# Kernel optimization log

Hardware: AMD Instinct MI355X
Metric: run time of the kernel (lower is better)

Reference implementation:

```python
import math
import jax, jax.numpy as jnp
import numpy as np

B, S, D = 4, 2048, 1024
H, HD = 16, 64
NUM_BUCKETS = 32
MAX_DISTANCE = 128
EPS = 1e-6
ENC_S = 512


def _relative_position_bucket(relative_position):
    # bidirectional=False path
    num_buckets = NUM_BUCKETS
    rp = -jnp.minimum(relative_position, 0)  # [S, S] nonneg
    max_exact = num_buckets // 2
    is_small = rp < max_exact
    scale = (num_buckets - max_exact) / math.log(MAX_DISTANCE / max_exact)
    large = max_exact + (jnp.log(jnp.maximum(rp, 1).astype(jnp.float32) / max_exact) * scale).astype(jnp.int32)
    large = jnp.minimum(large, num_buckets - 1)
    return jnp.where(is_small, rp, large)


def compute_bias(rel_emb, q_len, k_len):
    ctx = jnp.arange(q_len)[:, None]
    mem = jnp.arange(k_len)[None, :]
    bucket = _relative_position_bucket(mem - ctx)          # [q, k] int
    values = rel_emb[bucket]                                # [q, k, H]
    return jnp.transpose(values, (2, 0, 1))[None]           # [1, H, q, k]


def setup_inputs() -> dict:
    key = jax.random.key(0)
    ks = jax.random.split(key, 8)
    std = 0.02
    return {
        "input_ids": jax.random.normal(ks[0], (B, S, D), jnp.float32),
        "encoder_output": jax.random.normal(ks[1], (B, ENC_S, D), jnp.float32),
        "wq": jax.random.normal(ks[2], (D, H * HD), jnp.float32) * std,
        "wk": jax.random.normal(ks[3], (D, H * HD), jnp.float32) * std,
        "wv": jax.random.normal(ks[4], (D, H * HD), jnp.float32) * std,
        "wo": jax.random.normal(ks[5], (H * HD, D), jnp.float32) * std,
        "rel_emb": jax.random.normal(ks[6], (NUM_BUCKETS, H), jnp.float32) * std,
        "ln_w": jnp.ones((D,), jnp.float32),
    }


def reference(input_ids, encoder_output, wq, wk, wv, wo, rel_emb, ln_w):
    origin = input_ids
    # MT5LayerNorm: RMS norm, no mean subtraction, no bias
    variance = jnp.mean(jnp.square(input_ids.astype(jnp.float32)), axis=-1, keepdims=True)
    x = (input_ids * jax.lax.rsqrt(variance + EPS)) * ln_w

    q = (x @ wq).reshape(B, S, H, HD)
    k = (x @ wk).reshape(B, S, H, HD)
    v = (x @ wv).reshape(B, S, H, HD)

    # NOTE: T5-style attention has no 1/sqrt(d) scaling
    scores = jnp.einsum("bqhd,bkhd->bhqk", q, k)
    scores = scores + compute_bias(rel_emb, S, S)
    attn = jax.nn.softmax(scores, axis=-1)
    ctx = jnp.einsum("bhqk,bkhd->bqhd", attn, v).reshape(B, S, H * HD)
    attn_out = ctx @ wo

    # residual connection (dropout is identity at rate 0 / eval)
    return origin + attn_out
```

## Files before the change

### kernel.cpp

```cpp
#include <hip/hip_runtime.h>
#include <hip/hip_bf16.h>
#include <math.h>

#define S_LEN 2048
#define D_DIM 1024
#define NHEAD 16

typedef __attribute__((ext_vector_type(8))) short bf16x8;
typedef __attribute__((ext_vector_type(4))) float floatx4;

__device__ __forceinline__ short f32_bf16(float f) {
  union { float f; unsigned u; } v; v.f = f;
  unsigned r = v.u + 0x7FFFu + ((v.u >> 16) & 1u);
  return (short)(r >> 16);
}

__device__ __forceinline__ float exp2_fast(float x) {
#if __has_builtin(__builtin_amdgcn_exp2f)
  return __builtin_amdgcn_exp2f(x);
#else
  float r; asm("v_exp_f32 %0, %1" : "=v"(r) : "v"(x)); return r;
#endif
}

__device__ __forceinline__ void gload16(const void* g, void* l) {
  __builtin_amdgcn_global_load_lds((const __attribute__((address_space(1))) unsigned*)g,
                                   (__attribute__((address_space(3))) unsigned*)l,
                                   16, 0, 0);
}

__global__ __launch_bounds__(256) void prep_k(const float* __restrict__ x,
                                              const float* __restrict__ lnw,
                                              const float* __restrict__ wq,
                                              const float* __restrict__ wk,
                                              const float* __restrict__ wv,
                                              const float* __restrict__ wo,
                                              short* __restrict__ xb,
                                              short* __restrict__ oqkv,
                                              short* __restrict__ owo) {
  if (blockIdx.x < 8192) {
    int row = blockIdx.x;
    const float4* xr = (const float4*)(x + (size_t)row * D_DIM);
    float4 v = xr[threadIdx.x];
    float ss = v.x*v.x + v.y*v.y + v.z*v.z + v.w*v.w;
    #pragma unroll
    for (int off = 32; off > 0; off >>= 1) ss += __shfl_xor(ss, off);
    __shared__ float red[4];
    if ((threadIdx.x & 63) == 0) red[threadIdx.x >> 6] = ss;
    __syncthreads();
    float scale = rsqrtf((red[0]+red[1]+red[2]+red[3]) * (1.f/D_DIM) + 1e-6f);
    float4 wv4 = ((const float4*)lnw)[threadIdx.x];
    short4 o;
    o.x = f32_bf16(v.x*scale*wv4.x);
    o.y = f32_bf16(v.y*scale*wv4.y);
    o.z = f32_bf16(v.z*scale*wv4.z);
    o.w = f32_bf16(v.w*scale*wv4.w);
    ((short4*)xb)[(size_t)row*256 + threadIdx.x] = o;
  } else {
    __shared__ float tile[64][65];
    int id = blockIdx.x - 8192;
    int m  = id >> 8;
    int tt = id & 255;
    int tn = tt >> 4, tk = tt & 15;
    const float* src = (m == 0) ? wq : (m == 1) ? wk : (m == 2) ? wv : wo;
    float scale = (m == 0) ? 1.44269504f : 1.0f;
    int t = threadIdx.x;
    int kl  = t >> 4;
    int nl4 = t & 15;
    #pragma unroll
    for (int i = 0; i < 4; i++) {
      int k = i*16 + kl;
      float4 v = *(const float4*)&src[(size_t)(tk*64 + k)*1024 + tn*64 + nl4*4];
      tile[k][nl4*4+0] = v.x;
      tile[k][nl4*4+1] = v.y;
      tile[k][nl4*4+2] = v.z;
      tile[k][nl4*4+3] = v.w;
    }
    __syncthreads();
    short* dst = (m < 3) ? oqkv : owo;
    size_t nbase = (m < 3) ? (size_t)m * 1024 : 0;
    #pragma unroll
    for (int i = 0; i < 2; i++) {
      int idx = i*256 + t;
      int nl = idx >> 3;
      int g  = idx & 7;
      short tmp[8];
      #pragma unroll
      for (int j = 0; j < 8; j++) tmp[j] = f32_bf16(tile[g*8 + j][nl] * scale);
      *(bf16x8*)&dst[(nbase + tn*64 + nl)*1024 + tk*64 + g*8] = *(bf16x8*)tmp;
    }
  }
}

template<bool WRITE_VT>
__global__ __launch_bounds__(512, 2) void gemm256(const short* __restrict__ A,
                                                  const short* __restrict__ Bt,
                                                  short* __restrict__ Cb,
                                                  short* __restrict__ vt,
                                                  int N, int K, int NBN) {
  __shared__ __align__(16) short As[4][256*32];
  __shared__ __align__(16) short Bs[4][256*32];
  const int tid = threadIdx.x;
  const int w = tid >> 6, lane = tid & 63, quad = lane >> 4, l16 = lane & 15;
  const int wm = w >> 2, wn = w & 3;
  const int id = blockIdx.x;
  const int o = (id & 7) * (gridDim.x >> 3) + (id >> 3);
  const int bm = o / NBN, bn = o % NBN;
  const short* Ag = A  + (size_t)bm * 256 * K;
  const short* Bg = Bt + (size_t)bn * 256 * K;
  const int r4 = lane >> 2, c4 = lane & 3;
  const int lc  = c4 ^ ((r4 >> 1) & 3);
  const int swz = (quad ^ ((l16 >> 1) & 3)) * 8;

  floatx4 acc[8][4] = {};

  #define SA(t_) do {                                                          \
    gload16(Ag + (size_t)((w    )*16 + r4) * K + (size_t)(t_)*32 + lc*8,       \
            &As[(t_) & 3][(w    )*512]);                                       \
    gload16(Ag + (size_t)((w + 8)*16 + r4) * K + (size_t)(t_)*32 + lc*8,       \
            &As[(t_) & 3][(w + 8)*512]);                                       \
  } while (0)
  #define SB(t_) do {                                                          \
    gload16(Bg + (size_t)((w    )*16 + r4) * K + (size_t)(t_)*32 + lc*8,       \
            &Bs[(t_) & 3][(w    )*512]);                                       \
    gload16(Bg + (size_t)((w + 8)*16 + r4) * K + (size_t)(t_)*32 + lc*8,       \
            &Bs[(t_) & 3][(w + 8)*512]);                                       \
  } while (0)

  #define PH(t_, STG_, VMW_) do {                                              \
    const short* Ab = &As[(t_) & 3][0];                                        \
    const short* Bb = &Bs[(t_) & 3][0];                                        \
    bf16x8 af[8], bfr[4];                                                      \
    _Pragma("unroll")                                                          \
    for (int i = 0; i < 8; i++)                                                \
      af[i] = *(const bf16x8*)&Ab[(wm*128 + i*16 + l16)*32 + swz];             \
    bfr[0] = *(const bf16x8*)&Bb[(wn*64 +  0 + l16)*32 + swz];                 \
    bfr[1] = *(const bf16x8*)&Bb[(wn*64 + 16 + l16)*32 + swz];                 \
    if (STG_) SA((t_) + 3);                                                    \
    asm volatile("s_waitcnt lgkmcnt(0)");                                      \
    __builtin_amdgcn_sched_barrier(0);                                         \
    __builtin_amdgcn_s_setprio(1);                                             \
    _Pragma("unroll")                                                          \
    for (int i = 0; i < 8; i++) {                                              \
      acc[i][0] = __builtin_amdgcn_mfma_f32_16x16x32_bf16(af[i], bfr[0], acc[i][0], 0, 0, 0); \
      acc[i][1] = __builtin_amdgcn_mfma_f32_16x16x32_bf16(af[i], bfr[1], acc[i][1], 0, 0, 0); \
    }                                                                          \
    __builtin_amdgcn_s_setprio(0);                                             \
    bfr[2] = *(const bf16x8*)&Bb[(wn*64 + 32 + l16)*32 + swz];                 \
    bfr[3] = *(const bf16x8*)&Bb[(wn*64 + 48 + l16)*32 + swz];                 \
    if (STG_) SB((t_) + 3);                                                    \
    asm volatile("s_waitcnt lgkmcnt(0)");                                      \
    __builtin_amdgcn_sched_barrier(0);                                         \
    __builtin_amdgcn_s_setprio(1);                                             \
    _Pragma("unroll")                                                          \
    for (int i = 0; i < 8; i++) {                                              \
      acc[i][2] = __builtin_amdgcn_mfma_f32_16x16x32_bf16(af[i], bfr[2], acc[i][2], 0, 0, 0); \
      acc[i][3] = __builtin_amdgcn_mfma_f32_16x16x32_bf16(af[i], bfr[3], acc[i][3], 0, 0, 0); \
    }                                                                          \
    __builtin_amdgcn_s_setprio(0);                                             \
    asm volatile("s_waitcnt " VMW_);                                           \
    __builtin_amdgcn_s_barrier();                                              \
    __builtin_amdgcn_sched_barrier(0);                                         \
  } while (0)

  SA(0); SB(0); SA(1); SB(1); SA(2); SB(2);
  asm volatile("s_waitcnt vmcnt(8)");
  __builtin_amdgcn_s_barrier();
  __builtin_amdgcn_sched_barrier(0);

  #pragma unroll 1
  for (int t = 0; t < 29; ++t) PH(t, true, "vmcnt(8)");
  PH(29, false, "vmcnt(4)");
  PH(30, false, "vmcnt(0)");
  PH(31, false, "vmcnt(0)");
  #undef SA
  #undef SB
  #undef PH

  if (WRITE_VT && (bn*256 + wn*64) >= 2048) {
    #pragma unroll
    for (int i = 0; i < 8; i++) {
      int row0 = bm*256 + wm*128 + i*16 + quad*4;
      int b = row0 >> 11, s = row0 & 2047;
      #pragma unroll
      for (int j = 0; j < 4; j++) {
        int hcol = bn*256 + wn*64 + j*16 + l16 - 2048;
        short4 st;
        st.x = f32_bf16(acc[i][j][0]);
        st.y = f32_bf16(acc[i][j][1]);
        st.z = f32_bf16(acc[i][j][2]);
        st.w = f32_bf16(acc[i][j][3]);
        int bh = (b << 4) + (hcol >> 6);
        *(short4*)&vt[((size_t)(bh*64 + (hcol & 63)))*2048 + s] = st;
      }
    }
    return;
  }

  #pragma unroll
  for (int i = 0; i < 8; i++) {
    int row0 = bm*256 + wm*128 + i*16 + quad*4;
    #pragma unroll
    for (int j = 0; j < 4; j++) {
      int col = bn*256 + wn*64 + j*16 + l16;
      #pragma unroll
      for (int r = 0; r < 4; r++)
        Cb[(size_t)(row0 + r) * N + col] = f32_bf16(acc[i][j][r]);
    }
  }
}

template<bool ADD_RES, int PANELS>
__global__ __launch_bounds__(256) void gemm_bt(const short* __restrict__ A,
                                               const short* __restrict__ Bt,
                                               short* __restrict__ Cb,
                                               float* __restrict__ Cf,
                                               const float* __restrict__ res,
                                               int M, int N, int K) {
  constexpr int BK = 32;
  __shared__ __align__(16) short As[2][128*BK];
  __shared__ __align__(16) short Bs[2][128*BK];
  int tid = threadIdx.x;
  int w = tid >> 6, lane = tid & 63, quad = lane >> 4, l16 = lane & 15;
  int wr = w >> 1, wc = w & 1;
  const int id = blockIdx.x;
  const int xcd = id & 7, g = id >> 3;
  const int bm = g / PANELS;
  const int bn = xcd * PANELS + (g % PANELS);
  const short* Ag = A + (size_t)bm * 128 * K;
  const short* Bg = Bt + (size_t)bn * 128 * K;
  const int r4 = lane >> 2;
  const int c4 = lane & 3;
  const int lc = c4 ^ ((r4 >> 1) & 3);
  const int swz = (quad ^ ((l16 >> 1) & 3)) * 8;

  floatx4 acc[4][4] = {};

  #define GSTAGE(p_, k0_) do {                                                  \
    _Pragma("unroll")                                                           \
    for (int i = 0; i < 2; i++) {                                               \
      int c = w + i*4;                                                          \
      gload16(Ag + (size_t)(c*16 + r4) * K + (k0_) + lc*8, &As[p_][c*16*BK]);   \
      gload16(Bg + (size_t)(c*16 + r4) * K + (k0_) + lc*8, &Bs[p_][c*16*BK]);   \
    }                                                                           \
  } while (0)

  GSTAGE(0, 0);
  int p = 0;
  for (int k0 = 0; k0 < K; k0 += BK) {
    __syncthreads();
    if (k0 + BK < K) GSTAGE(p ^ 1, k0 + BK);
    bf16x8 af[4], bfr[4];
    #pragma unroll
    for (int i = 0; i < 4; i++) {
      af[i]  = *(const bf16x8*)&As[p][(wr*64 + i*16 + l16)*BK + swz];
      bfr[i] = *(const bf16x8*)&Bs[p][(wc*64 + i*16 + l16)*BK + swz];
    }
    #pragma unroll
    for (int i = 0; i < 4; i++)
      #pragma unroll
      for (int j = 0; j < 4; j++)
        acc[i][j] = __builtin_amdgcn_mfma_f32_16x16x32_bf16(af[i], bfr[j], acc[i][j], 0, 0, 0);
    p ^= 1;
  }
  #undef GSTAGE

  #pragma unroll
  for (int i = 0; i < 4; i++) {
    int row0 = bm*128 + wr*64 + i*16 + quad*4;
    #pragma unroll
    for (int j = 0; j < 4; j++) {
      int col = bn*128 + wc*64 + j*16 + l16;
      #pragma unroll
      for (int r = 0; r < 4; r++) {
        size_t idx = (size_t)(row0 + r) * N + col;
        if (ADD_RES) Cf[idx] = res[idx] + acc[i][j][r];
        else         Cb[idx] = f32_bf16(acc[i][j][r]);
      }
    }
  }
}

__global__ __launch_bounds__(512) void flash_k(const short* __restrict__ qkv,
                                               const short* __restrict__ vt,
                                               const float* __restrict__ rel_emb,
                                               short* __restrict__ ctx) {
  __shared__ __align__(16) short Kb[2][64*64];
  __shared__ __align__(16) short Vb[2][64*64];
  __shared__ float lut2[132];

  const int L = blockIdx.x + 8*blockIdx.y;
  const int xcd = L & 7, kk_ = L >> 3;
  const int bh = xcd*8 + (kk_ >> 3);
  const int qt = kk_ & 7;
  const int b = bh >> 4, h = bh & 15;
  const int t = threadIdx.x, w = t >> 6, lane = t & 63, quad = lane >> 4, l16 = lane & 15;
  const float L2E = 1.44269504f;

  if (t < 129) {
    int rp = t, bucket;
    if (rp < 16) bucket = rp;
    else {
      bucket = 16 + (int)(logf((float)rp * 0.0625f) * (16.f / logf(8.f)));
      if (bucket > 31) bucket = 31;
    }
    lut2[t] = rel_emb[bucket*16 + h] * L2E;
  }
  const float bfut  = rel_emb[h] * L2E;
  const float bpast = rel_emb[31*16 + h] * L2E;
  const floatx4 bf4 = {bfut, bfut, bfut, bfut};
  const floatx4 bp4 = {bpast, bpast, bpast, bpast};
  const floatx4 zz4 = {0.f, 0.f, 0.f, 0.f};

  const int srow = lane >> 3;
  const int slc  = (lane & 7) ^ srow;
  const int rho  = w*8 + srow;
  const int kperm = 32*(rho >> 5) + 8*((rho >> 2) & 3) + 4*((rho >> 4) & 1) + (rho & 3);

  const short* kgU = qkv + ((size_t)b*S_LEN)*3072 + 1024 + h*64;
  const int    loK = kperm*3072 + slc*8;
  const short* vgU = vt + ((size_t)bh*64)*2048;
  const int    loV = rho*2048 + slc*8;

  bf16x8 qB[2][2];
  #pragma unroll
  for (int rb = 0; rb < 2; rb++) {
    const short* qb = qkv + ((size_t)(b*S_LEN + qt*256 + rb*128 + w*16 + l16))*3072 + h*64;
    qB[rb][0] = *(const bf16x8*)&qb[quad*8];
    qB[rb][1] = *(const bf16x8*)&qb[32 + quad*8];
  }

  floatx4 o[2][4] = {};
  floatx4 li4[2] = {};
  const short ONE = (short)0x3F80;
  bf16x8 onesA = {ONE, ONE, ONE, ONE, ONE, ONE, ONE, ONE};

  const int swz0 = (quad     ^ (l16 & 7)) * 8;
  const int swz1 = ((quad+4) ^ (l16 & 7)) * 8;

  #define STAGE(P_, KT_) do {                                                   \
    const short* ka_ = kgU + (size_t)(KT_)*196608 + loK;                        \
    gload16(ka_, &Kb[P_][(w*8)*64]);                                            \
    const short* va_ = vgU + loV + (KT_)*64;                                    \
    gload16(va_, &Vb[P_][(w*8)*64]);                                            \
  } while (0)

  #define BODY(P_, KT_) do {                                                    \
    __syncthreads();                                                            \
    if ((KT_) < 31) STAGE((P_) ^ 1, (KT_) + 1);                                 \
    bool boundary = ((KT_) >= 4*qt - 2) && ((KT_) <= 4*qt + 3);                 \
    floatx4 cinit = boundary ? zz4 : (((KT_) >= 4*qt) ? bf4 : bp4);             \
    floatx4 sc[2][4];                                                           \
    _Pragma("unroll")                                                           \
    for (int c = 0; c < 4; c++) {                                               \
      int rowA = (c*16 + l16)*64;                                               \
      bf16x8 ka0 = *(const bf16x8*)&Kb[P_][rowA + swz0];                        \
      bf16x8 ka1 = *(const bf16x8*)&Kb[P_][rowA + swz1];                        \
      _Pragma("unroll")                                                         \
      for (int rb = 0; rb < 2; rb++) {                                          \
        floatx4 z = __builtin_amdgcn_mfma_f32_16x16x32_bf16(ka0, qB[rb][0], cinit, 0, 0, 0); \
        z = __builtin_amdgcn_mfma_f32_16x16x32_bf16(ka1, qB[rb][1], z, 0, 0, 0);\
        sc[rb][c] = z;                                                          \
      }                                                                         \
    }                                                                           \
    if (boundary) {                                                             \
      _Pragma("unroll")                                                         \
      for (int rb = 0; rb < 2; rb++) {                                          \
        int q0 = qt*256 + rb*128 + w*16 + l16;                                  \
        _Pragma("unroll")                                                       \
        for (int c = 0; c < 4; c++) {                                           \
          int kk = (KT_)*64 + 32*(c >> 1) + 8*quad + 4*(c & 1);                 \
          _Pragma("unroll")                                                     \
          for (int r = 0; r < 4; r++) {                                         \
            int d = q0 - (kk + r);                                              \
            d = d < 0 ? 0 : (d > 128 ? 128 : d);                                \
            sc[rb][c][r] += lut2[d];                                            \
          }                                                                     \
        }                                                                       \
      }                                                                         \
    }                                                                           \
    _Pragma("unroll")                                                           \
    for (int rb = 0; rb < 2; rb++)                                              \
      _Pragma("unroll")                                                         \
      for (int c = 0; c < 4; c++)                                               \
        _Pragma("unroll")                                                       \
        for (int r = 0; r < 4; r++)                                             \
          sc[rb][c][r] = exp2_fast(sc[rb][c][r]);                               \
    bf16x8 pf[2][2];                                                            \
    _Pragma("unroll")                                                           \
    for (int rb = 0; rb < 2; rb++) {                                            \
      _Pragma("unroll")                                                         \
      for (int hh = 0; hh < 2; hh++) {                                          \
        union { bf16x8 v; unsigned u[4]; } pk;                                  \
        floatx4 a = sc[rb][2*hh], bb = sc[rb][2*hh + 1];                        \
        pk.u[0] = __builtin_amdgcn_perm(__float_as_uint(a[1]),  __float_as_uint(a[0]),  0x07060302); \
        pk.u[1] = __builtin_amdgcn_perm(__float_as_uint(a[3]),  __float_as_uint(a[2]),  0x07060302); \
        pk.u[2] = __builtin_amdgcn_perm(__float_as_uint(bb[1]), __float_as_uint(bb[0]), 0x07060302); \
        pk.u[3] = __builtin_amdgcn_perm(__float_as_uint(bb[3]), __float_as_uint(bb[2]), 0x07060302); \
        pf[rb][hh] = pk.v;                                                      \
      }                                                                         \
    }                                                                           \
    _Pragma("unroll")                                                           \
    for (int rb = 0; rb < 2; rb++) {                                            \
      li4[rb] = __builtin_amdgcn_mfma_f32_16x16x32_bf16(onesA, pf[rb][0], li4[rb], 0, 0, 0); \
      li4[rb] = __builtin_amdgcn_mfma_f32_16x16x32_bf16(onesA, pf[rb][1], li4[rb], 0, 0, 0); \
    }                                                                           \
    _Pragma("unroll")                                                           \
    for (int jj = 0; jj < 4; jj++) {                                            \
      int rowV = (jj*16 + l16)*64;                                              \
      bf16x8 va0 = *(const bf16x8*)&Vb[P_][rowV + swz0];                        \
      bf16x8 va1 = *(const bf16x8*)&Vb[P_][rowV + swz1];                        \
      _Pragma("unroll")                                                         \
      for (int rb = 0; rb < 2; rb++) {                                          \
        o[rb][jj] = __builtin_amdgcn_mfma_f32_16x16x32_bf16(va0, pf[rb][0], o[rb][jj], 0, 0, 0); \
        o[rb][jj] = __builtin_amdgcn_mfma_f32_16x16x32_bf16(va1, pf[rb][1], o[rb][jj], 0, 0, 0); \
      }                                                                         \
    }                                                                           \
  } while (0)

  STAGE(0, 0);
  for (int kt = 0; kt < 32; kt += 2) {
    BODY(0, kt);
    BODY(1, kt + 1);
  }

  #pragma unroll
  for (int rb = 0; rb < 2; rb++) {
    float inv = 1.f / li4[rb][0];
    size_t row = (size_t)(b*S_LEN + qt*256 + rb*128 + w*16 + l16);
    #pragma unroll
    for (int jj = 0; jj < 4; jj++) {
      short4 st;
      st.x = f32_bf16(o[rb][jj][0] * inv);
      st.y = f32_bf16(o[rb][jj][1] * inv);
      st.z = f32_bf16(o[rb][jj][2] * inv);
      st.w = f32_bf16(o[rb][jj][3] * inv);
      *(short4*)&ctx[row*1024 + h*64 + jj*16 + quad*4] = st;
    }
  }
  #undef STAGE
  #undef BODY
}

extern "C" void kernel_launch(void* const* d_in, const int* in_sizes, int n_in,
                              void* d_out, int out_size, void* d_ws, size_t ws_size,
                              hipStream_t stream) {
  const float* input_ids = (const float*)d_in[0];
  const float* wq      = (const float*)d_in[2];
  const float* wk      = (const float*)d_in[3];
  const float* wv      = (const float*)d_in[4];
  const float* wo      = (const float*)d_in[5];
  const float* rel_emb = (const float*)d_in[6];
  const float* ln_w    = (const float*)d_in[7];
  float* out = (float*)d_out;

  char* ws = (char*)d_ws;
  short* xb     = (short*)ws;  ws += (size_t)8192*1024*2;
  short* wqkv_t = (short*)ws;  ws += (size_t)3072*1024*2;
  short* wo_t   = (short*)ws;  ws += (size_t)1024*1024*2;
  short* qkv    = (short*)ws;  ws += (size_t)8192*3072*2;
  short* vt     = (short*)ws;  ws += (size_t)64*64*2048*2;
  short* ctx    = (short*)ws;  ws += (size_t)8192*1024*2;

  prep_k<<<8192 + 1024, 256, 0, stream>>>(input_ids, ln_w, wq, wk, wv, wo,
                                          xb, wqkv_t, wo_t);
  gemm256<true><<<384, 512, 0, stream>>>(xb, wqkv_t, qkv, vt, 3072, 1024, 12);
  flash_k<<<dim3(8, 64), 512, 0, stream>>>(qkv, vt, rel_emb, ctx);
  gemm_bt<true, 1><<<512, 256, 0, stream>>>(ctx, wo_t, nullptr, out, input_ids,
                                            8192, 1024, 1024);
}
```

Measured before the change: 284.0 us.

## Shrink gemm256 to 256x128 tiles, reuse it for output projection, software-pipeline PV

The QKV GEMM tile narrows from 256x256 to 256x128, doubling the grid to 768 blocks and halving B-side shared memory and accumulators. The same kernel, with a residual-add epilogue, replaces the separate 128x128 output-projection GEMM. In the flash kernel, P·V for tile k-1 now runs while tile k's softmax is produced, using a third V buffer and a final drain step, so exp/pack work overlaps with MFMA. Costs are more A-tile reloads, extra registers for the previous P fragments, and a triple-buffer rotation that adds bookkeeping.

```diff
diff --git a/kernel.cpp b/kernel.cpp
--- a/kernel.cpp
+++ b/kernel.cpp
@@ -92,71 +92,65 @@
   }
 }
 
-template<bool WRITE_VT>
-__global__ __launch_bounds__(512, 2) void gemm256(const short* __restrict__ A,
-                                                  const short* __restrict__ Bt,
-                                                  short* __restrict__ Cb,
-                                                  short* __restrict__ vt,
-                                                  int N, int K, int NBN) {
+template<bool WRITE_VT, bool ADD_RES>
+__global__ __launch_bounds__(512) void gemm256(const short* __restrict__ A,
+                                               const short* __restrict__ Bt,
+                                               short* __restrict__ Cb,
+                                               float* __restrict__ Cf,
+                                               const float* __restrict__ res,
+                                               short* __restrict__ vt,
+                                               int N, int NBN) {
   __shared__ __align__(16) short As[4][256*32];
-  __shared__ __align__(16) short Bs[4][256*32];
+  __shared__ __align__(16) short Bs[4][128*32];
   const int tid = threadIdx.x;
   const int w = tid >> 6, lane = tid & 63, quad = lane >> 4, l16 = lane & 15;
   const int wm = w >> 2, wn = w & 3;
   const int id = blockIdx.x;
   const int o = (id & 7) * (gridDim.x >> 3) + (id >> 3);
   const int bm = o / NBN, bn = o % NBN;
-  const short* Ag = A  + (size_t)bm * 256 * K;
-  const short* Bg = Bt + (size_t)bn * 256 * K;
+  const short* Ag = A  + (size_t)bm * 256 * 1024;
+  const short* Bg = Bt + (size_t)bn * 128 * 1024;
   const int r4 = lane >> 2, c4 = lane & 3;
   const int lc  = c4 ^ ((r4 >> 1) & 3);
   const int swz = (quad ^ ((l16 >> 1) & 3)) * 8;
 
-  floatx4 acc[8][4] = {};
+  floatx4 acc[8][2] = {};
 
   #define SA(t_) do {                                                          \
-    gload16(Ag + (size_t)((w    )*16 + r4) * K + (size_t)(t_)*32 + lc*8,       \
+    gload16(Ag + (size_t)((w    )*16 + r4) * 1024 + (t_)*32 + lc*8,            \
             &As[(t_) & 3][(w    )*512]);                                       \
-    gload16(Ag + (size_t)((w + 8)*16 + r4) * K + (size_t)(t_)*32 + lc*8,       \
+    gload16(Ag + (size_t)((w + 8)*16 + r4) * 1024 + (t_)*32 + lc*8,            \
             &As[(t_) & 3][(w + 8)*512]);                                       \
   } while (0)
   #define SB(t_) do {                                                          \
-    gload16(Bg + (size_t)((w    )*16 + r4) * K + (size_t)(t_)*32 + lc*8,       \
+    gload16(Bg + (size_t)((w    )*16 + r4) * 1024 + (t_)*32 + lc*8,            \
             &Bs[(t_) & 3][(w    )*512]);                                       \
-    gload16(Bg + (size_t)((w + 8)*16 + r4) * K + (size_t)(t_)*32 + lc*8,       \
-            &Bs[(t_) & 3][(w + 8)*512]);                                       \
   } while (0)
 
   #define PH(t_, STG_, VMW_) do {                                              \
     const short* Ab = &As[(t_) & 3][0];                                        \
     const short* Bb = &Bs[(t_) & 3][0];                                        \
-    bf16x8 af[8], bfr[4];                                                      \
+    bf16x8 af[8], bf0, bf1;                                                    \
     _Pragma("unroll")                                                          \
     for (int i = 0; i < 8; i++)                                                \
       af[i] = *(const bf16x8*)&Ab[(wm*128 + i*16 + l16)*32 + swz];             \
-    bfr[0] = *(const bf16x8*)&Bb[(wn*64 +  0 + l16)*32 + swz];                 \
-    bfr[1] = *(const bf16x8*)&Bb[(wn*64 + 16 + l16)*32 + swz];                 \
+    bf0 = *(const bf16x8*)&Bb[(wn*32 +  0 + l16)*32 + swz];                    \
     if (STG_) SA((t_) + 3);                                                    \
     asm volatile("s_waitcnt lgkmcnt(0)");                                      \
     __builtin_amdgcn_sched_barrier(0);                                         \
     __builtin_amdgcn_s_setprio(1);                                             \
     _Pragma("unroll")                                                          \
-    for (int i = 0; i < 8; i++) {                                              \
-      acc[i][0] = __builtin_amdgcn_mfma_f32_16x16x32_bf16(af[i], bfr[0], acc[i][0], 0, 0, 0); \
-      acc[i][1] = __builtin_amdgcn_mfma_f32_16x16x32_bf16(af[i], bfr[1], acc[i][1], 0, 0, 0); \
-    }                                                                          \
+    for (int i = 0; i < 8; i++)                                                \
+      acc[i][0] = __builtin_amdgcn_mfma_f32_16x16x32_bf16(af[i], bf0, acc[i][0], 0, 0, 0); \
     __builtin_amdgcn_s_setprio(0);                                             \
-    bfr[2] = *(const bf16x8*)&Bb[(wn*64 + 32 + l16)*32 + swz];                 \
-    bfr[3] = *(const bf16x8*)&Bb[(wn*64 + 48 + l16)*32 + swz];                 \
+    bf1 = *(const bf16x8*)&Bb[(wn*32 + 16 + l16)*32 + swz];                    \
     if (STG_) SB((t_) + 3);                                                    \
     asm volatile("s_waitcnt lgkmcnt(0)");                                      \
     __builtin_amdgcn_sched_barrier(0);                                         \
     __builtin_amdgcn_s_setprio(1);                                             \
     _Pragma("unroll")                                                          \
-    for (int i = 0; i < 8; i++) {                                              \
-      acc[i][2] = __builtin_amdgcn_mfma_f32_16x16x32_bf16(af[i], bfr[2], acc[i][2], 0, 0, 0); \
-      acc[i][3] = __builtin_amdgcn_mfma_f32_16x16x32_bf16(af[i], bfr[3], acc[i][3], 0, 0, 0); \
-    }                                                                          \
+    for (int i = 0; i < 8; i++)                                                \
+      acc[i][1] = __builtin_amdgcn_mfma_f32_16x16x32_bf16(af[i], bf1, acc[i][1], 0, 0, 0); \
     __builtin_amdgcn_s_setprio(0);                                             \
     asm volatile("s_waitcnt " VMW_);                                           \
     __builtin_amdgcn_s_barrier();                                              \
@@ -164,27 +158,27 @@
   } while (0)
 
   SA(0); SB(0); SA(1); SB(1); SA(2); SB(2);
-  asm volatile("s_waitcnt vmcnt(8)");
+  asm volatile("s_waitcnt vmcnt(6)");
   __builtin_amdgcn_s_barrier();
   __builtin_amdgcn_sched_barrier(0);
 
   #pragma unroll 1
-  for (int t = 0; t < 29; ++t) PH(t, true, "vmcnt(8)");
-  PH(29, false, "vmcnt(4)");
+  for (int t = 0; t < 29; ++t) PH(t, true, "vmcnt(6)");
+  PH(29, false, "vmcnt(3)");
   PH(30, false, "vmcnt(0)");
   PH(31, false, "vmcnt(0)");
   #undef SA
   #undef SB
   #undef PH
 
-  if (WRITE_VT && (bn*256 + wn*64) >= 2048) {
+  if (WRITE_VT && bn >= 16) {
     #pragma unroll
     for (int i = 0; i < 8; i++) {
       int row0 = bm*256 + wm*128 + i*16 + quad*4;
       int b = row0 >> 11, s = row0 & 2047;
       #pragma unroll
-      for (int j = 0; j < 4; j++) {
-        int hcol = bn*256 + wn*64 + j*16 + l16 - 2048;
+      for (int j = 0; j < 2; j++) {
+        int hcol = (bn - 16)*128 + wn*32 + j*16 + l16;
         short4 st;
         st.x = f32_bf16(acc[i][j][0]);
         st.y = f32_bf16(acc[i][j][1]);
@@ -201,76 +195,8 @@
   for (int i = 0; i < 8; i++) {
     int row0 = bm*256 + wm*128 + i*16 + quad*4;
     #pragma unroll
-    for (int j = 0; j < 4; j++) {
-      int col = bn*256 + wn*64 + j*16 + l16;
-      #pragma unroll
-      for (int r = 0; r < 4; r++)
-        Cb[(size_t)(row0 + r) * N + col] = f32_bf16(acc[i][j][r]);
-    }
-  }
-}
-
-template<bool ADD_RES, int PANELS>
-__global__ __launch_bounds__(256) void gemm_bt(const short* __restrict__ A,
-                                               const short* __restrict__ Bt,
-                                               short* __restrict__ Cb,
-                                               float* __restrict__ Cf,
-                                               const float* __restrict__ res,
-                                               int M, int N, int K) {
-  constexpr int BK = 32;
-  __shared__ __align__(16) short As[2][128*BK];
-  __shared__ __align__(16) short Bs[2][128*BK];
-  int tid = threadIdx.x;
-  int w = tid >> 6, lane = tid & 63, quad = lane >> 4, l16 = lane & 15;
-  int wr = w >> 1, wc = w & 1;
-  const int id = blockIdx.x;
-  const int xcd = id & 7, g = id >> 3;
-  const int bm = g / PANELS;
-  const int bn = xcd * PANELS + (g % PANELS);
-  const short* Ag = A + (size_t)bm * 128 * K;
-  const short* Bg = Bt + (size_t)bn * 128 * K;
-  const int r4 = lane >> 2;
-  const int c4 = lane & 3;
-  const int lc = c4 ^ ((r4 >> 1) & 3);
-  const int swz = (quad ^ ((l16 >> 1) & 3)) * 8;
-
-  floatx4 acc[4][4] = {};
-
-  #define GSTAGE(p_, k0_) do {                                                  \
-    _Pragma("unroll")                                                           \
-    for (int i = 0; i < 2; i++) {                                               \
-      int c = w + i*4;                                                          \
-      gload16(Ag + (size_t)(c*16 + r4) * K + (k0_) + lc*8, &As[p_][c*16*BK]);   \
-      gload16(Bg + (size_t)(c*16 + r4) * K + (k0_) + lc*8, &Bs[p_][c*16*BK]);   \
-    }                                                                           \
-  } while (0)
-
-  GSTAGE(0, 0);
-  int p = 0;
-  for (int k0 = 0; k0 < K; k0 += BK) {
-    __syncthreads();
-    if (k0 + BK < K) GSTAGE(p ^ 1, k0 + BK);
-    bf16x8 af[4], bfr[4];
-    #pragma unroll
-    for (int i = 0; i < 4; i++) {
-      af[i]  = *(const bf16x8*)&As[p][(wr*64 + i*16 + l16)*BK + swz];
-      bfr[i] = *(const bf16x8*)&Bs[p][(wc*64 + i*16 + l16)*BK + swz];
-    }
-    #pragma unroll
-    for (int i = 0; i < 4; i++)
-      #pragma unroll
-      for (int j = 0; j < 4; j++)
-        acc[i][j] = __builtin_amdgcn_mfma_f32_16x16x32_bf16(af[i], bfr[j], acc[i][j], 0, 0, 0);
-    p ^= 1;
-  }
-  #undef GSTAGE
-
-  #pragma unroll
-  for (int i = 0; i < 4; i++) {
-    int row0 = bm*128 + wr*64 + i*16 + quad*4;
-    #pragma unroll
-    for (int j = 0; j < 4; j++) {
-      int col = bn*128 + wc*64 + j*16 + l16;
+    for (int j = 0; j < 2; j++) {
+      int col = bn*128 + wn*32 + j*16 + l16;
       #pragma unroll
       for (int r = 0; r < 4; r++) {
         size_t idx = (size_t)(row0 + r) * N + col;
@@ -286,7 +212,7 @@
                                                const float* __restrict__ rel_emb,
                                                short* __restrict__ ctx) {
   __shared__ __align__(16) short Kb[2][64*64];
-  __shared__ __align__(16) short Vb[2][64*64];
+  __shared__ __align__(16) short Vb[3][64*64];
   __shared__ float lut2[132];
 
   const int L = blockIdx.x + 8*blockIdx.y;
@@ -322,6 +248,11 @@
   const short* vgU = vt + ((size_t)bh*64)*2048;
   const int    loV = rho*2048 + slc*8;
 
+  {
+    bf16x8 z = {};
+    *(bf16x8*)&Vb[2][t*8] = z;
+  }
+
   bf16x8 qB[2][2];
   #pragma unroll
   for (int rb = 0; rb < 2; rb++) {
@@ -334,20 +265,24 @@
   floatx4 li4[2] = {};
   const short ONE = (short)0x3F80;
   bf16x8 onesA = {ONE, ONE, ONE, ONE, ONE, ONE, ONE, ONE};
+  bf16x8 pfP[2][2] = {};
 
   const int swz0 = (quad     ^ (l16 & 7)) * 8;
   const int swz1 = ((quad+4) ^ (l16 & 7)) * 8;
 
-  #define STAGE(P_, KT_) do {                                                   \
+  int vnext = 1;
+  int vprev = 2;
+
+  #define STAGE_T(KP_, VN_, KT_) do {                                           \
     const short* ka_ = kgU + (size_t)(KT_)*196608 + loK;                        \
-    gload16(ka_, &Kb[P_][(w*8)*64]);                                            \
+    gload16(ka_, &Kb[KP_][(w*8)*64]);                                           \
     const short* va_ = vgU + loV + (KT_)*64;                                    \
-    gload16(va_, &Vb[P_][(w*8)*64]);                                            \
+    gload16(va_, &Vb[VN_][(w*8)*64]);                                           \
   } while (0)
 
   #define BODY(P_, KT_) do {                                                    \
     __syncthreads();                                                            \
-    if ((KT_) < 31) STAGE((P_) ^ 1, (KT_) + 1);                                 \
+    if ((KT_) < 31) STAGE_T((P_) ^ 1, vnext, (KT_) + 1);                        \
     bool boundary = ((KT_) >= 4*qt - 2) && ((KT_) <= 4*qt + 3);                 \
     floatx4 cinit = boundary ? zz4 : (((KT_) >= 4*qt) ? bf4 : bp4);             \
     floatx4 sc[2][4];                                                           \
@@ -386,7 +321,7 @@
         _Pragma("unroll")                                                       \
         for (int r = 0; r < 4; r++)                                             \
           sc[rb][c][r] = exp2_fast(sc[rb][c][r]);                               \
-    bf16x8 pf[2][2];                                                            \
+    bf16x8 pfL[2][2];                                                           \
     _Pragma("unroll")                                                           \
     for (int rb = 0; rb < 2; rb++) {                                            \
       _Pragma("unroll")                                                         \
@@ -397,31 +332,51 @@
         pk.u[1] = __builtin_amdgcn_perm(__float_as_uint(a[3]),  __float_as_uint(a[2]),  0x07060302); \
         pk.u[2] = __builtin_amdgcn_perm(__float_as_uint(bb[1]), __float_as_uint(bb[0]), 0x07060302); \
         pk.u[3] = __builtin_amdgcn_perm(__float_as_uint(bb[3]), __float_as_uint(bb[2]), 0x07060302); \
-        pf[rb][hh] = pk.v;                                                      \
+        pfL[rb][hh] = pk.v;                                                     \
       }                                                                         \
     }                                                                           \
-    _Pragma("unroll")                                                           \
-    for (int rb = 0; rb < 2; rb++) {                                            \
-      li4[rb] = __builtin_amdgcn_mfma_f32_16x16x32_bf16(onesA, pf[rb][0], li4[rb], 0, 0, 0); \
-      li4[rb] = __builtin_amdgcn_mfma_f32_16x16x32_bf16(onesA, pf[rb][1], li4[rb], 0, 0, 0); \
-    }                                                                           \
+                 \
     _Pragma("unroll")                                                           \
     for (int jj = 0; jj < 4; jj++) {                                            \
       int rowV = (jj*16 + l16)*64;                                              \
-      bf16x8 va0 = *(const bf16x8*)&Vb[P_][rowV + swz0];                        \
-      bf16x8 va1 = *(const bf16x8*)&Vb[P_][rowV + swz1];                        \
+      bf16x8 va0 = *(const bf16x8*)&Vb[vprev][rowV + swz0];                     \
+      bf16x8 va1 = *(const bf16x8*)&Vb[vprev][rowV + swz1];                     \
       _Pragma("unroll")                                                         \
       for (int rb = 0; rb < 2; rb++) {                                          \
-        o[rb][jj] = __builtin_amdgcn_mfma_f32_16x16x32_bf16(va0, pf[rb][0], o[rb][jj], 0, 0, 0); \
-        o[rb][jj] = __builtin_amdgcn_mfma_f32_16x16x32_bf16(va1, pf[rb][1], o[rb][jj], 0, 0, 0); \
+        o[rb][jj] = __builtin_amdgcn_mfma_f32_16x16x32_bf16(va0, pfP[rb][0], o[rb][jj], 0, 0, 0); \
+        o[rb][jj] = __builtin_amdgcn_mfma_f32_16x16x32_bf16(va1, pfP[rb][1], o[rb][jj], 0, 0, 0); \
       }                                                                         \
     }                                                                           \
+    _Pragma("unroll")                                                           \
+    for (int rb = 0; rb < 2; rb++) {                                            \
+      li4[rb] = __builtin_amdgcn_mfma_f32_16x16x32_bf16(onesA, pfL[rb][0], li4[rb], 0, 0, 0); \
+      li4[rb] = __builtin_amdgcn_mfma_f32_16x16x32_bf16(onesA, pfL[rb][1], li4[rb], 0, 0, 0); \
+    }                                                                           \
+    _Pragma("unroll")                                                           \
+    for (int rb = 0; rb < 2; rb++) {                                            \
+      pfP[rb][0] = pfL[rb][0];                                                  \
+      pfP[rb][1] = pfL[rb][1];                                                  \
+    }                                                                           \
+    vprev = (vprev == 2) ? 0 : vprev + 1;                                       \
+    vnext = (vnext == 2) ? 0 : vnext + 1;                                       \
   } while (0)
 
-  STAGE(0, 0);
+  STAGE_T(0, 0, 0);
   for (int kt = 0; kt < 32; kt += 2) {
     BODY(0, kt);
     BODY(1, kt + 1);
+  }
+
+  #pragma unroll
+  for (int jj = 0; jj < 4; jj++) {
+    int rowV = (jj*16 + l16)*64;
+    bf16x8 va0 = *(const bf16x8*)&Vb[vprev][rowV + swz0];
+    bf16x8 va1 = *(const bf16x8*)&Vb[vprev][rowV + swz1];
+    #pragma unroll
+    for (int rb = 0; rb < 2; rb++) {
+      o[rb][jj] = __builtin_amdgcn_mfma_f32_16x16x32_bf16(va0, pfP[rb][0], o[rb][jj], 0, 0, 0);
+      o[rb][jj] = __builtin_amdgcn_mfma_f32_16x16x32_bf16(va1, pfP[rb][1], o[rb][jj], 0, 0, 0);
+    }
   }
 
   #pragma unroll
@@ -438,7 +393,7 @@
       *(short4*)&ctx[row*1024 + h*64 + jj*16 + quad*4] = st;
     }
   }
-  #undef STAGE
+  #undef STAGE_T
   #undef BODY
 }
 
@@ -464,8 +419,9 @@
 
   prep_k<<<8192 + 1024, 256, 0, stream>>>(input_ids, ln_w, wq, wk, wv, wo,
                                           xb, wqkv_t, wo_t);
-  gemm256<true><<<384, 512, 0, stream>>>(xb, wqkv_t, qkv, vt, 3072, 1024, 12);
+  gemm256<true, false><<<768, 512, 0, stream>>>(xb, wqkv_t, qkv, nullptr,
+                                                nullptr, vt, 3072, 24);
   flash_k<<<dim3(8, 64), 512, 0, stream>>>(qkv, vt, rel_emb, ctx);
-  gemm_bt<true, 1><<<512, 256, 0, stream>>>(ctx, wo_t, nullptr, out, input_ids,
-                                            8192, 1024, 1024);
-}
+  gemm256<false, true><<<256, 512, 0, stream>>>(ctx, wo_t, nullptr, out,
+                                                input_ids, nullptr, 1024, 8);
+}
```

Result: no change. 288.3 us (+1.5%).
